# Kernel tuning notes

Hardware: AMD Instinct MI355X
Metric: run time of the kernel (lower is better)

The kernel has to match this reference:

```python
import jax, jax.numpy as jnp
import numpy as np

N = 8192
DISCO_LAMBDA = 0.1
DCORR_POWER = 2  # static, from __init__


def setup_inputs() -> dict:
    key = jax.random.key(0)
    k1, k2, k3, k4 = jax.random.split(key, 4)
    inferences = jax.random.uniform(k1, (N,), dtype=jnp.float32, minval=1e-6, maxval=1.0 - 1e-6)
    labels = jax.random.randint(k2, (N,), 0, 2, dtype=jnp.int32)
    disco_target = jax.random.normal(k3, (N,), dtype=jnp.float32)
    weights = jax.random.uniform(k4, (N,), dtype=jnp.float32)
    return {"inferences": inferences, "labels": labels,
            "disco_target": disco_target, "weights": weights}


def _bce(p, y, w):
    # torch F.binary_cross_entropy: clamps log terms at -100, mean reduction
    logp = jnp.clip(jnp.log(p), -100.0)
    log1mp = jnp.clip(jnp.log1p(-p), -100.0)
    return jnp.mean(w * -(y * logp + (1.0 - y) * log1mp))


def _dcorr(v1, v2, w, mask):
    # mask selects labels==0 subset; zero weights + divide by subset count
    # reproduces torch means over the fancy-indexed subset exactly.
    nf = jnp.sum(mask)                      # subset size (traced scalar)
    wm = w * mask                           # [N]
    amat = jnp.abs(v1[:, None] - v1[None, :])   # [N,N]
    bmat = jnp.abs(v2[:, None] - v2[None, :])   # [N,N]
    a_row = (amat @ wm) / nf                # weighted row means
    b_row = (bmat @ wm) / nf
    a_tot = jnp.dot(a_row, wm) / nf
    b_tot = jnp.dot(b_row, wm) / nf
    Amat = amat - a_row[None, :] - a_row[:, None] + a_tot  # double-centered
    Bmat = bmat - b_row[None, :] - b_row[:, None] + b_tot
    AB = jnp.dot((Amat * Bmat) @ wm, wm) / (nf * nf)
    AA = jnp.dot((Amat * Amat) @ wm, wm) / (nf * nf)
    BB = jnp.dot((Bmat * Bmat) @ wm, wm) / (nf * nf)
    if DCORR_POWER == 1:
        return AB / jnp.sqrt(AA * BB)
    elif DCORR_POWER == 2:
        return AB ** 2 / (AA * BB)
    else:
        return (AB / jnp.sqrt(AA * BB)) ** DCORR_POWER


def reference(inferences, labels, disco_target, weights):
    y = labels.astype(inferences.dtype)
    bce = _bce(inferences, y, weights)
    mask = (labels == 0).astype(inferences.dtype)
    dcorr = _dcorr(inferences, disco_target, weights, mask)
    total = bce + DISCO_LAMBDA * dcorr
    return (total, bce, DISCO_LAMBDA * dcorr)
```

## Files before the change

kernel.cpp:

```cpp
#include <hip/hip_runtime.h>
#include <math.h>

constexpr int N_ELEM = 8192;
constexpr int BLK    = 256;
constexpr int K1_GRID = N_ELEM / BLK;
constexpr int WAVES_PER_BLK = 4;
constexpr int ROWS_PER_WAVE = 2;
constexpr int ROWS_PER_BLK  = WAVES_PER_BLK * ROWS_PER_WAVE;
constexpr int K2_GRID = N_ELEM / ROWS_PER_BLK;
constexpr float LAMBDA = 0.1f;

constexpr size_t OFF_GPART = 2048;
constexpr size_t OFF_C     = 51200;

__global__ void __launch_bounds__(BLK) k1_init(
        const float* __restrict__ inf, const int* __restrict__ lab,
        const float* __restrict__ tgt, const float* __restrict__ wt,
        double* __restrict__ part, float4* __restrict__ c) {
    __shared__ float red[WAVES_PER_BLK][8];
    int tx = threadIdx.x;
    int lane = tx & 63, wid = tx >> 6;
    int i = blockIdx.x * BLK + tx;

    float p = inf[i];
    int   y = lab[i];
    float w = wt[i];
    float t = tgt[i];

    float logp   = fmaxf(logf(p),    -100.0f);
    float log1mp = fmaxf(log1pf(-p), -100.0f);
    float yf = (float)y;
    float bce = w * -(yf * logp + (1.0f - yf) * log1mp);

    bool  m  = (y == 0);
    float mf = m ? 1.0f : 0.0f;
    float wm = m ? w : 0.0f;

    c[i] = make_float4(p, t, wm, 0.0f);

    float v[7] = {bce, mf, wm, wm * p, wm * p * p, wm * t, wm * t * t};
#pragma unroll
    for (int k = 0; k < 7; ++k) {
        float s = v[k];
#pragma unroll
        for (int d = 32; d > 0; d >>= 1) s += __shfl_xor(s, d);
        if (lane == 0) red[wid][k] = s;
    }
    __syncthreads();
    if (tx < 7) {
        double s = (double)red[0][tx] + (double)red[1][tx]
                 + (double)red[2][tx] + (double)red[3][tx];
        part[blockIdx.x * 8 + tx] = s;
    }
}

__global__ void __launch_bounds__(BLK) k2_pairs(
        const float4* __restrict__ c, double* __restrict__ gpart) {
    __shared__ double sred[WAVES_PER_BLK][6];
    int tx = threadIdx.x, lane = tx & 63, wid = tx >> 6;
    int r0 = blockIdx.x * ROWS_PER_BLK + wid * ROWS_PER_WAVE;

    float4 c0 = c[r0], c1 = c[r0 + 1];
    float x0 = c0.x, y0 = c0.y, x1 = c1.x, y1 = c1.y;

    float ra0 = 0.f, rb0 = 0.f, pp0 = 0.f;
    float ra1 = 0.f, rb1 = 0.f, pp1 = 0.f;
#pragma unroll 4
    for (int jj = 0; jj < N_ELEM / 64; ++jj) {
        float4 cj = c[jj * 64 + lane];
        float u = cj.z;
        float d0 = x0 - cj.x, e0 = y0 - cj.y;
        ra0 = fmaf(u, fabsf(d0), ra0);
        rb0 = fmaf(u, fabsf(e0), rb0);
        pp0 = fmaf(u, fabsf(d0) * fabsf(e0), pp0);
        float d1 = x1 - cj.x, e1 = y1 - cj.y;
        ra1 = fmaf(u, fabsf(d1), ra1);
        rb1 = fmaf(u, fabsf(e1), rb1);
        pp1 = fmaf(u, fabsf(d1) * fabsf(e1), pp1);
    }
#pragma unroll
    for (int d = 32; d > 0; d >>= 1) {
        ra0 += __shfl_xor(ra0, d); rb0 += __shfl_xor(rb0, d); pp0 += __shfl_xor(pp0, d);
        ra1 += __shfl_xor(ra1, d); rb1 += __shfl_xor(rb1, d); pp1 += __shfl_xor(pp1, d);
    }
    if (lane == 0) {
        double u0 = (double)c0.z, u1 = (double)c1.z;
        double A0 = (double)ra0, B0 = (double)rb0, P0 = (double)pp0;
        double A1 = (double)ra1, B1 = (double)rb1, P1 = (double)pp1;
        sred[wid][0] = u0 * P0 + u1 * P1;
        sred[wid][1] = u0 * A0 + u1 * A1;
        sred[wid][2] = u0 * A0 * A0 + u1 * A1 * A1;
        sred[wid][3] = u0 * B0 + u1 * B1;
        sred[wid][4] = u0 * B0 * B0 + u1 * B1 * B1;
        sred[wid][5] = u0 * A0 * B0 + u1 * A1 * B1;
    }
    __syncthreads();
    if (tx == 0) {
        double* g = gpart + (size_t)blockIdx.x * 6;
#pragma unroll
        for (int k = 0; k < 6; ++k)
            g[k] = sred[0][k] + sred[1][k] + sred[2][k] + sred[3][k];
    }
}

__global__ void __launch_bounds__(BLK) k3_final(
        const double* __restrict__ part, const double* __restrict__ gpart,
        float* __restrict__ out) {
    __shared__ double dred[WAVES_PER_BLK][6];
    int tx = threadIdx.x, lane = tx & 63, wid = tx >> 6;

    double acc[6] = {0, 0, 0, 0, 0, 0};
    for (int r = tx; r < K2_GRID; r += BLK) {
        const double* g = gpart + (size_t)r * 6;
#pragma unroll
        for (int k = 0; k < 6; ++k) acc[k] += g[k];
    }
#pragma unroll
    for (int k = 0; k < 6; ++k) {
        double s = acc[k];
#pragma unroll
        for (int d = 32; d > 0; d >>= 1) s += __shfl_xor(s, d);
        if (lane == 0) dred[wid][k] = s;
    }
    __syncthreads();
    if (tx == 0) {
        double P   = dred[0][0] + dred[1][0] + dred[2][0] + dred[3][0];
        double Ra1 = dred[0][1] + dred[1][1] + dred[2][1] + dred[3][1];
        double Ra2 = dred[0][2] + dred[1][2] + dred[2][2] + dred[3][2];
        double Rb1 = dred[0][3] + dred[1][3] + dred[2][3] + dred[3][3];
        double Rb2 = dred[0][4] + dred[1][4] + dred[2][4] + dred[3][4];
        double Rab = dred[0][5] + dred[1][5] + dred[2][5] + dred[3][5];

        double bceS = 0, NF = 0, W = 0, S1a = 0, S2a = 0, S1b = 0, S2b = 0;
        for (int b = 0; b < K1_GRID; ++b) {
            const double* pb = part + b * 8;
            bceS += pb[0]; NF += pb[1]; W += pb[2];
            S1a += pb[3]; S2a += pb[4]; S1b += pb[5]; S2b += pb[6];
        }

        double nf = NF;
        double in1 = 1.0 / nf;
        double in2 = in1 * in1, in3 = in2 * in1, in4 = in2 * in2;

        double AAa = 2.0 * (W * S2a - S1a * S1a)
                   - 4.0 * Ra2 * in1 + 2.0 * W * Ra2 * in2
                   + 4.0 * Ra1 * Ra1 * in2 - 4.0 * W * Ra1 * Ra1 * in3
                   + W * W * Ra1 * Ra1 * in4;
        double BBa = 2.0 * (W * S2b - S1b * S1b)
                   - 4.0 * Rb2 * in1 + 2.0 * W * Rb2 * in2
                   + 4.0 * Rb1 * Rb1 * in2 - 4.0 * W * Rb1 * Rb1 * in3
                   + W * W * Rb1 * Rb1 * in4;
        double ABa = P
                   - 4.0 * Rab * in1 + 2.0 * W * Rab * in2
                   + 4.0 * Ra1 * Rb1 * in2 - 4.0 * W * Ra1 * Rb1 * in3
                   + W * W * Ra1 * Rb1 * in4;

        double AB = ABa * in2, AA = AAa * in2, BB = BBa * in2;
        double dcorr = (AB * AB) / (AA * BB);
        double ld = (double)LAMBDA * dcorr;
        double bce = bceS / (double)N_ELEM;
        out[0] = (float)(bce + ld);
        out[1] = (float)bce;
        out[2] = (float)ld;
    }
}

extern "C" void kernel_launch(void* const* d_in, const int* in_sizes, int n_in,
                              void* d_out, int out_size, void* d_ws, size_t ws_size,
                              hipStream_t stream) {
    const float* inf = (const float*)d_in[0];
    const int*   lab = (const int*)d_in[1];
    const float* tgt = (const float*)d_in[2];
    const float* wt  = (const float*)d_in[3];
    float* out = (float*)d_out;

    double* part  = (double*)d_ws;
    double* gpart = (double*)((char*)d_ws + OFF_GPART);
    float4* c     = (float4*)((char*)d_ws + OFF_C);

    k1_init<<<K1_GRID, BLK, 0, stream>>>(inf, lab, tgt, wt, part, c);
    k2_pairs<<<K2_GRID, BLK, 0, stream>>>(c, gpart);
    k3_final<<<1, BLK, 0, stream>>>(part, gpart, out);
}
```

Before: 85.91 us.

## Drop init kernel; read raw inputs in pair kernel and fold moments into final

```diff
diff --git a/kernel.cpp b/kernel.cpp
--- a/kernel.cpp
+++ b/kernel.cpp
@@ -3,77 +3,40 @@
 
 constexpr int N_ELEM = 8192;
 constexpr int BLK    = 256;
-constexpr int K1_GRID = N_ELEM / BLK;
 constexpr int WAVES_PER_BLK = 4;
 constexpr int ROWS_PER_WAVE = 2;
 constexpr int ROWS_PER_BLK  = WAVES_PER_BLK * ROWS_PER_WAVE;
-constexpr int K2_GRID = N_ELEM / ROWS_PER_BLK;
+constexpr int KP_GRID = N_ELEM / ROWS_PER_BLK;
+constexpr int BLKF    = 1024;
 constexpr float LAMBDA = 0.1f;
 
-constexpr size_t OFF_GPART = 2048;
-constexpr size_t OFF_C     = 51200;
 
-__global__ void __launch_bounds__(BLK) k1_init(
+__global__ void __launch_bounds__(BLK) kp_pairs(
         const float* __restrict__ inf, const int* __restrict__ lab,
         const float* __restrict__ tgt, const float* __restrict__ wt,
-        double* __restrict__ part, float4* __restrict__ c) {
-    __shared__ float red[WAVES_PER_BLK][8];
-    int tx = threadIdx.x;
-    int lane = tx & 63, wid = tx >> 6;
-    int i = blockIdx.x * BLK + tx;
-
-    float p = inf[i];
-    int   y = lab[i];
-    float w = wt[i];
-    float t = tgt[i];
-
-    float logp   = fmaxf(logf(p),    -100.0f);
-    float log1mp = fmaxf(log1pf(-p), -100.0f);
-    float yf = (float)y;
-    float bce = w * -(yf * logp + (1.0f - yf) * log1mp);
-
-    bool  m  = (y == 0);
-    float mf = m ? 1.0f : 0.0f;
-    float wm = m ? w : 0.0f;
-
-    c[i] = make_float4(p, t, wm, 0.0f);
-
-    float v[7] = {bce, mf, wm, wm * p, wm * p * p, wm * t, wm * t * t};
-#pragma unroll
-    for (int k = 0; k < 7; ++k) {
-        float s = v[k];
-#pragma unroll
-        for (int d = 32; d > 0; d >>= 1) s += __shfl_xor(s, d);
-        if (lane == 0) red[wid][k] = s;
-    }
-    __syncthreads();
-    if (tx < 7) {
-        double s = (double)red[0][tx] + (double)red[1][tx]
-                 + (double)red[2][tx] + (double)red[3][tx];
-        part[blockIdx.x * 8 + tx] = s;
-    }
-}
-
-__global__ void __launch_bounds__(BLK) k2_pairs(
-        const float4* __restrict__ c, double* __restrict__ gpart) {
+        double* __restrict__ gpart) {
     __shared__ double sred[WAVES_PER_BLK][6];
     int tx = threadIdx.x, lane = tx & 63, wid = tx >> 6;
     int r0 = blockIdx.x * ROWS_PER_BLK + wid * ROWS_PER_WAVE;
 
-    float4 c0 = c[r0], c1 = c[r0 + 1];
-    float x0 = c0.x, y0 = c0.y, x1 = c1.x, y1 = c1.y;
+    float x0 = inf[r0],     y0 = tgt[r0];
+    float x1 = inf[r0 + 1], y1 = tgt[r0 + 1];
+    float u0 = (lab[r0]     == 0) ? wt[r0]     : 0.0f;
+    float u1 = (lab[r0 + 1] == 0) ? wt[r0 + 1] : 0.0f;
 
     float ra0 = 0.f, rb0 = 0.f, pp0 = 0.f;
     float ra1 = 0.f, rb1 = 0.f, pp1 = 0.f;
 #pragma unroll 4
     for (int jj = 0; jj < N_ELEM / 64; ++jj) {
-        float4 cj = c[jj * 64 + lane];
-        float u = cj.z;
-        float d0 = x0 - cj.x, e0 = y0 - cj.y;
+        int j = jj * 64 + lane;
+        float xj = inf[j], yj = tgt[j], wj = wt[j];
+        int   lj = lab[j];
+        float u = (lj == 0) ? wj : 0.0f;
+        float d0 = x0 - xj, e0 = y0 - yj;
         ra0 = fmaf(u, fabsf(d0), ra0);
         rb0 = fmaf(u, fabsf(e0), rb0);
         pp0 = fmaf(u, fabsf(d0) * fabsf(e0), pp0);
-        float d1 = x1 - cj.x, e1 = y1 - cj.y;
+        float d1 = x1 - xj, e1 = y1 - yj;
         ra1 = fmaf(u, fabsf(d1), ra1);
         rb1 = fmaf(u, fabsf(e1), rb1);
         pp1 = fmaf(u, fabsf(d1) * fabsf(e1), pp1);
@@ -84,15 +47,15 @@
         ra1 += __shfl_xor(ra1, d); rb1 += __shfl_xor(rb1, d); pp1 += __shfl_xor(pp1, d);
     }
     if (lane == 0) {
-        double u0 = (double)c0.z, u1 = (double)c1.z;
+        double U0 = (double)u0, U1 = (double)u1;
         double A0 = (double)ra0, B0 = (double)rb0, P0 = (double)pp0;
         double A1 = (double)ra1, B1 = (double)rb1, P1 = (double)pp1;
-        sred[wid][0] = u0 * P0 + u1 * P1;
-        sred[wid][1] = u0 * A0 + u1 * A1;
-        sred[wid][2] = u0 * A0 * A0 + u1 * A1 * A1;
-        sred[wid][3] = u0 * B0 + u1 * B1;
-        sred[wid][4] = u0 * B0 * B0 + u1 * B1 * B1;
-        sred[wid][5] = u0 * A0 * B0 + u1 * A1 * B1;
+        sred[wid][0] = U0 * P0 + U1 * P1;
+        sred[wid][1] = U0 * A0 + U1 * A1;
+        sred[wid][2] = U0 * A0 * A0 + U1 * A1 * A1;
+        sred[wid][3] = U0 * B0 + U1 * B1;
+        sred[wid][4] = U0 * B0 * B0 + U1 * B1 * B1;
+        sred[wid][5] = U0 * A0 * B0 + U1 * A1 * B1;
     }
     __syncthreads();
     if (tx == 0) {
@@ -103,43 +66,72 @@
     }
 }
 
-__global__ void __launch_bounds__(BLK) k3_final(
-        const double* __restrict__ part, const double* __restrict__ gpart,
-        float* __restrict__ out) {
-    __shared__ double dred[WAVES_PER_BLK][6];
+__global__ void __launch_bounds__(BLKF) kf_final(
+        const float* __restrict__ inf, const int* __restrict__ lab,
+        const float* __restrict__ tgt, const float* __restrict__ wt,
+        const double* __restrict__ gpart, float* __restrict__ out) {
+    __shared__ float  redM[BLKF / 64][8];
+    __shared__ double redG[BLKF / 64][6];
     int tx = threadIdx.x, lane = tx & 63, wid = tx >> 6;
 
-    double acc[6] = {0, 0, 0, 0, 0, 0};
-    for (int r = tx; r < K2_GRID; r += BLK) {
-        const double* g = gpart + (size_t)r * 6;
+    float vb = 0.f, vn = 0.f, vw = 0.f, v1a = 0.f, v2a = 0.f, v1b = 0.f, v2b = 0.f;
 #pragma unroll
-        for (int k = 0; k < 6; ++k) acc[k] += g[k];
+    for (int k = 0; k < N_ELEM / BLKF; ++k) {
+        int i = k * BLKF + tx;
+        float p = inf[i];
+        int   y = lab[i];
+        float w = wt[i];
+        float t = tgt[i];
+        float logp   = fmaxf(logf(p),    -100.0f);
+        float log1mp = fmaxf(log1pf(-p), -100.0f);
+        float yf = (float)y;
+        vb += w * -(yf * logp + (1.0f - yf) * log1mp);
+        bool  m  = (y == 0);
+        float mf = m ? 1.0f : 0.0f;
+        float wm = m ? w : 0.0f;
+        vn += mf; vw += wm;
+        v1a += wm * p; v2a += wm * p * p;
+        v1b += wm * t; v2b += wm * t * t;
+    }
+    float vm[7] = {vb, vn, vw, v1a, v2a, v1b, v2b};
+#pragma unroll
+    for (int k = 0; k < 7; ++k) {
+        float s = vm[k];
+#pragma unroll
+        for (int d = 32; d > 0; d >>= 1) s += __shfl_xor(s, d);
+        if (lane == 0) redM[wid][k] = s;
+    }
+
+    double a0, a1, a2, a3, a4, a5;
+    {
+        const double* g = gpart + (size_t)tx * 6;
+        a0 = g[0]; a1 = g[1]; a2 = g[2]; a3 = g[3]; a4 = g[4]; a5 = g[5];
     }
 #pragma unroll
-    for (int k = 0; k < 6; ++k) {
-        double s = acc[k];
-#pragma unroll
-        for (int d = 32; d > 0; d >>= 1) s += __shfl_xor(s, d);
-        if (lane == 0) dred[wid][k] = s;
+    for (int d = 32; d > 0; d >>= 1) {
+        a0 += __shfl_xor(a0, d); a1 += __shfl_xor(a1, d); a2 += __shfl_xor(a2, d);
+        a3 += __shfl_xor(a3, d); a4 += __shfl_xor(a4, d); a5 += __shfl_xor(a5, d);
+    }
+    if (lane == 0) {
+        redG[wid][0] = a0; redG[wid][1] = a1; redG[wid][2] = a2;
+        redG[wid][3] = a3; redG[wid][4] = a4; redG[wid][5] = a5;
     }
     __syncthreads();
+
     if (tx == 0) {
-        double P   = dred[0][0] + dred[1][0] + dred[2][0] + dred[3][0];
-        double Ra1 = dred[0][1] + dred[1][1] + dred[2][1] + dred[3][1];
-        double Ra2 = dred[0][2] + dred[1][2] + dred[2][2] + dred[3][2];
-        double Rb1 = dred[0][3] + dred[1][3] + dred[2][3] + dred[3][3];
-        double Rb2 = dred[0][4] + dred[1][4] + dred[2][4] + dred[3][4];
-        double Rab = dred[0][5] + dred[1][5] + dred[2][5] + dred[3][5];
+        double M[7] = {0, 0, 0, 0, 0, 0, 0};
+        double G[6] = {0, 0, 0, 0, 0, 0};
+        for (int wv = 0; wv < BLKF / 64; ++wv) {
+#pragma unroll
+            for (int k = 0; k < 7; ++k) M[k] += (double)redM[wv][k];
+#pragma unroll
+            for (int k = 0; k < 6; ++k) G[k] += redG[wv][k];
+        }
+        double bceS = M[0], NF = M[1], W = M[2];
+        double S1a = M[3], S2a = M[4], S1b = M[5], S2b = M[6];
+        double P = G[0], Ra1 = G[1], Ra2 = G[2], Rb1 = G[3], Rb2 = G[4], Rab = G[5];
 
-        double bceS = 0, NF = 0, W = 0, S1a = 0, S2a = 0, S1b = 0, S2b = 0;
-        for (int b = 0; b < K1_GRID; ++b) {
-            const double* pb = part + b * 8;
-            bceS += pb[0]; NF += pb[1]; W += pb[2];
-            S1a += pb[3]; S2a += pb[4]; S1b += pb[5]; S2b += pb[6];
-        }
-
-        double nf = NF;
-        double in1 = 1.0 / nf;
+        double in1 = 1.0 / NF;
         double in2 = in1 * in1, in3 = in2 * in1, in4 = in2 * in2;
 
         double AAa = 2.0 * (W * S2a - S1a * S1a)
@@ -173,12 +165,8 @@
     const float* tgt = (const float*)d_in[2];
     const float* wt  = (const float*)d_in[3];
     float* out = (float*)d_out;
+    double* gpart = (double*)d_ws;
 
-    double* part  = (double*)d_ws;
-    double* gpart = (double*)((char*)d_ws + OFF_GPART);
-    float4* c     = (float4*)((char*)d_ws + OFF_C);
-
-    k1_init<<<K1_GRID, BLK, 0, stream>>>(inf, lab, tgt, wt, part, c);
-    k2_pairs<<<K2_GRID, BLK, 0, stream>>>(c, gpart);
-    k3_final<<<1, BLK, 0, stream>>>(part, gpart, out);
+    kp_pairs<<<KP_GRID, BLK, 0, stream>>>(inf, lab, tgt, wt, gpart);
+    kf_final<<<1, BLKF, 0, stream>>>(inf, lab, tgt, wt, gpart, out);
 }
```

New measurement: 92.71 us. 7.9% more time.
